# Optimization experiments

Measured on AMD Instinct MI355X. Metric: run time of the kernel, lower is better.

The kernel has to match this reference:

```python
import jax, jax.numpy as jnp
import numpy as np

EPS = 1e-8
LAMBDA_SOFTMAX = 9.0   # opt.lambda_softmax (SCAN t2i default)
ITERATION_STEP = 2     # opt.iteration_step
LEAKY_SLOPE = 0.1      # clipped_l2norm leaky relu slope


def l2norm(x, axis):
    norm = jnp.sqrt(jnp.sum(x * x, axis=axis, keepdims=True)) + EPS
    return x / norm


def cosine_sim(a, b, axis):
    w12 = jnp.sum(a * b, axis=axis)
    w1 = jnp.linalg.norm(a, axis=axis)
    w2 = jnp.linalg.norm(b, axis=axis)
    return w12 / jnp.clip(w1 * w2, EPS)


def func_attention_t2i(query, context):
    """query: [C, I, T, D] caption words per (caption, image) pair;
    context: [I, R, D] image regions. Returns weightedContext [C, I, T, D]."""
    # attn = bmm(context, query^T) -> [C, I, R, T]
    attn = jnp.einsum('ird,citd->cirt', context, query)
    # raw_feature_norm == 'clipped_l2norm': LeakyReLU(0.1) then l2norm over queryL
    attn = jax.nn.leaky_relu(attn, LEAKY_SLOPE)
    attn = l2norm(attn, axis=-1)
    # transpose -> [C, I, T, R]; temperature softmax over sourceL (regions)
    attn = jnp.swapaxes(attn, -1, -2)
    attn = jax.nn.softmax(attn * LAMBDA_SOFTMAX, axis=-1)
    # weightedContext = bmm(context^T, attn^T)^T -> [C, I, T, D]
    return jnp.einsum('citr,ird->citd', attn, context)


def setup_inputs() -> dict:
    key = jax.random.key(0)
    ks = jax.random.split(key, 4)
    B, R, T, D = 32, 36, 40, 1024
    # encoder outputs are l2-normalized along the feature dim
    img_emb = l2norm(jax.random.normal(ks[0], (B, R, D), jnp.float32), axis=-1)
    cap_emb = l2norm(jax.random.normal(ks[1], (B, T, D), jnp.float32), axis=-1)
    W_lin = jax.random.normal(ks[2], (2 * D, D), jnp.float32) * 0.02
    b_lin = jnp.zeros((D,), jnp.float32)
    W_gate = jax.random.normal(ks[3], (2 * D, D), jnp.float32) * 0.02
    b_gate = jnp.zeros((D,), jnp.float32)
    return dict(img_emb=img_emb, cap_emb=cap_emb,
                W_lin=W_lin, b_lin=b_lin, W_gate=W_gate, b_gate=b_gate)


def reference(img_emb, cap_emb, W_lin, b_lin, W_gate, b_gate):
    """xattn_score_Text_IMRAM (t2i) with gated memory, summed over iterations.
    Returns similarity score matrix [n_image, n_caption]."""
    C, T, D = cap_emb.shape
    I = img_emb.shape[0]
    # cap_i_expand: each caption repeated across all images
    cap_exp = jnp.broadcast_to(cap_emb[:, None], (C, I, T, D))
    query = cap_exp
    score = jnp.zeros((I, C), cap_emb.dtype)
    for _ in range(ITERATION_STEP):
        wc = func_attention_t2i(query, img_emb)            # [C, I, T, D]
        # cosine similarity per word vs original caption words, mean over words
        row_sim = cosine_sim(cap_exp, wc, axis=-1).mean(-1)  # [C, I]
        score = score + row_sim.T                           # [I, C]
        # gated_memory_t2i
        cat = jnp.concatenate([query, wc], axis=-1)         # [C, I, T, 2D]
        upd = jnp.tanh(cat @ W_lin + b_lin)
        gate = jax.nn.sigmoid(cat @ W_gate + b_gate)
        query = query * gate + upd * (1.0 - gate)
    return score
```

## Files before the change

kernel.cpp:

```cpp
#include <hip/hip_runtime.h>
#include <stdint.h>


typedef unsigned short u16;
typedef __attribute__((ext_vector_type(8))) short bf16x8;
typedef __attribute__((ext_vector_type(4))) float f32x4;

#define MFMA_BF16(a, b, c) __builtin_amdgcn_mfma_f32_16x16x32_bf16((a), (b), (c), 0, 0, 0)

__device__ __forceinline__ float bf2f(u16 u) {
  union { unsigned v; float f; } x; x.v = ((unsigned)u) << 16; return x.f;
}
__device__ __forceinline__ u16 f2bf(float f) {
  union { float f; unsigned v; } x; x.f = f;
  return (u16)((x.v + 0x7fffu + ((x.v >> 16) & 1u)) >> 16);
}
__device__ __forceinline__ float frcp(float x) { return __builtin_amdgcn_rcpf(x); }
__device__ __forceinline__ void gl2lds16(const u16* g, u16* l) {
  __builtin_amdgcn_global_load_lds((const __attribute__((address_space(1))) void*)g,
                                   (__attribute__((address_space(3))) void*)l, 16, 0, 0);
}

__global__ void prep_k(const float* __restrict__ img, const float* __restrict__ cap,
                       const float* __restrict__ Wl, const float* __restrict__ Wg,
                       u16* __restrict__ imgb, u16* __restrict__ capb,
                       u16* __restrict__ WTl, u16* __restrict__ WTg,
                       float* __restrict__ cnorm, u16* __restrict__ cwT0) {
  __shared__ u16 tile[32][33];
  const int b = blockIdx.x, tid = threadIdx.x;
  if (b < 2432) {
    const float* src; u16* dst; int idx;
    if (b < 1152) { src = img; dst = imgb; idx = (b * 256 + tid) * 4; }
    else { src = cap; dst = capb; idx = ((b - 1152) * 256 + tid) * 4; }
    const float4 v = *(const float4*)(src + idx);
    u16 o[4] = {f2bf(v.x), f2bf(v.y), f2bf(v.z), f2bf(v.w)};
    *(uint2*)(dst + idx) = *(const uint2*)o;
  } else if (b < 6528) {
    const int b2 = b - 2432;
    const int bx = b2 & 63, by = (b2 >> 6) & 31, bz = b2 >> 11;
    const float* src = bz ? Wg : Wl;
    u16* dst = bz ? WTg : WTl;
    const int k0 = bx * 32, n0 = by * 32;
    const int tx = tid & 31, ty = tid >> 5;
#pragma unroll
    for (int j = 0; j < 4; ++j)
      tile[ty + 8 * j][tx] = f2bf(src[(size_t)(k0 + ty + 8 * j) * 1024 + n0 + tx]);
    __syncthreads();
#pragma unroll
    for (int j = 0; j < 4; ++j)
      dst[(size_t)(n0 + ty + 8 * j) * 2048 + k0 + tx] = tile[tx][ty + 8 * j];
  } else if (b < 6848) {
    const int wv = tid >> 6, lane = tid & 63;
    const int row = (b - 6528) * 4 + wv;
    const float* p = cap + ((size_t)row << 10) + lane * 16;
    float s = 0.f;
#pragma unroll
    for (int e = 0; e < 16; ++e) { float v = p[e]; s += v * v; }
#pragma unroll
    for (int off = 32; off > 0; off >>= 1) s += __shfl_down(s, off, 64);
    if (lane == 0) cnorm[row] = sqrtf(s);
  } else {
    const int idx = ((b - 6848) * 256 + tid) * 8;
    uint4 z; z.x = z.y = z.z = z.w = 0u;
    *(uint4*)(cwT0 + idx) = z;
  }
}

__global__ __launch_bounds__(256, 2) void gemms_k(
    const u16* __restrict__ capb, const u16* __restrict__ imgb,
    const u16* __restrict__ WTl, const u16* __restrict__ WTg,
    u16* __restrict__ preL, u16* __restrict__ preG,
    u16* __restrict__ cwTL, u16* __restrict__ cwTG,
    const float* __restrict__ bL, const float* __restrict__ bG,
    float* __restrict__ S1, u16* __restrict__ Ghi, u16* __restrict__ Glo) {
  __shared__ __align__(16) char lsU[20480];
  const int bid = blockIdx.x;
  const int tid = threadIdx.x;
  const int wv = tid >> 6, lane = tid & 63;
  const int quad = lane >> 4, l15 = lane & 15;
  const bf16x8 zero8 = {0, 0, 0, 0, 0, 0, 0, 0};

  if (bid < 640) {
    u16* lsA = (u16*)lsU;
    u16* lsB = (u16*)(lsU + 4096);
    const int i = bid & 31, m0 = (bid >> 5) * 64;
    const u16* B = imgb + (size_t)i * 36 * 1024;
    f32x4 acc[3];
#pragma unroll
    for (int b = 0; b < 3; ++b) acc[b] = (f32x4){0.f, 0.f, 0.f, 0.f};
    for (int kt = 0; kt < 32; ++kt) {
      if (kt) __syncthreads();
      const int rr = tid >> 2, j = tid & 3;
      const int js = j ^ ((rr >> 2) & 3);
      gl2lds16(capb + (size_t)(m0 + rr) * 1024 + kt * 32 + js * 8,
               lsA + (size_t)(wv * 64) * 8);
      const int rc = rr < 36 ? rr : 35;
      gl2lds16(B + (size_t)rc * 1024 + kt * 32 + js * 8,
               lsB + (size_t)(wv * 64) * 8);
      __syncthreads();
      const int ra = wv * 16 + l15;
      const bf16x8 a2 = *(const bf16x8*)(lsA + ra * 32 + (quad ^ ((ra >> 2) & 3)) * 8);
      bf16x8 b3[3];
#pragma unroll
      for (int nf = 0; nf < 3; ++nf) {
        const int rb = nf * 16 + l15;
        const bf16x8 bv = *(const bf16x8*)(lsB + rb * 32 + (quad ^ ((rb >> 2) & 3)) * 8);
        b3[nf] = (rb < 36) ? bv : zero8;
      }
#pragma unroll
      for (int nf = 0; nf < 3; ++nf) acc[nf] = MFMA_BF16(a2, b3[nf], acc[nf]);
    }
#pragma unroll
    for (int nf = 0; nf < 3; ++nf)
#pragma unroll
      for (int rg = 0; rg < 4; ++rg) {
        const int m = m0 + wv * 16 + quad * 4 + rg;
        S1[((size_t)i * 1280 + m) * 48 + nf * 16 + l15] = acc[nf][rg];
      }
  } else if (bid < 944) {
    u16* lsA = (u16*)lsU;
    u16* lsBl = (u16*)(lsU + 4096);
    u16* lsBg = (u16*)(lsU + 12288);
    const int b2 = bid - 640;
    const int bm = b2 >> 3, bn = b2 & 7;
    const bool iscap = bm < 20;
    const u16* A = iscap ? capb + (size_t)bm * 64 * 1024
                         : imgb + (size_t)(bm - 20) * 64 * 1024;
    const int kofs = iscap ? 0 : 1024;
    const int wm = (wv & 1) * 32, wn = (wv >> 1) * 64;
    f32x4 accL[2][4], accG[2][4];
#pragma unroll
    for (int a = 0; a < 2; ++a)
#pragma unroll
      for (int b = 0; b < 4; ++b) {
        accL[a][b] = (f32x4){0.f, 0.f, 0.f, 0.f};
        accG[a][b] = (f32x4){0.f, 0.f, 0.f, 0.f};
      }
    for (int kt = 0; kt < 32; ++kt) {
      if (kt) __syncthreads();
      {
        const int row = tid >> 2, c8 = tid & 3;
        const int js = c8 ^ (row & 3);
        gl2lds16(A + (size_t)row * 1024 + kt * 32 + js * 8,
                 lsA + (size_t)(wv * 64) * 8);
      }
#pragma unroll
      for (int s = 0; s < 2; ++s) {
        const int idx = s * 256 + tid;
        const int row = idx >> 2, c8 = idx & 3;
        const int js = c8 ^ (row & 3);
        const size_t bro = (size_t)(bn * 128 + row) * 2048 + kofs + kt * 32 + js * 8;
        gl2lds16(WTl + bro, lsBl + (size_t)(s * 256 + wv * 64) * 8);
        gl2lds16(WTg + bro, lsBg + (size_t)(s * 256 + wv * 64) * 8);
      }
      __syncthreads();
      bf16x8 af[2], bl8[4], bg8[4];
#pragma unroll
      for (int mt = 0; mt < 2; ++mt) {
        const int ra = wm + mt * 16 + l15;
        af[mt] = *(const bf16x8*)(lsA + ra * 32 + (quad ^ (ra & 3)) * 8);
      }
#pragma unroll
      for (int nt = 0; nt < 4; ++nt) {
        const int rb = wn + nt * 16 + l15;
        const int off = rb * 32 + (quad ^ (rb & 3)) * 8;
        bl8[nt] = *(const bf16x8*)(lsBl + off);
        bg8[nt] = *(const bf16x8*)(lsBg + off);
      }
#pragma unroll
      for (int mt = 0; mt < 2; ++mt)
#pragma unroll
        for (int nt = 0; nt < 4; ++nt) {
          accL[mt][nt] = MFMA_BF16(af[mt], bl8[nt], accL[mt][nt]);
          accG[mt][nt] = MFMA_BF16(af[mt], bg8[nt], accG[mt][nt]);
        }
    }
#pragma unroll
    for (int mt = 0; mt < 2; ++mt)
#pragma unroll
      for (int nt = 0; nt < 4; ++nt) {
        const int n = bn * 128 + wn + nt * 16 + l15;
        if (iscap) {
          const float blv = bL[n], bgv = bG[n];
#pragma unroll
          for (int r = 0; r < 4; ++r) {
            const int m = bm * 64 + wm + mt * 16 + quad * 4 + r;
            preL[((size_t)m << 10) + n] = f2bf(accL[mt][nt][r] + blv);
            preG[((size_t)m << 10) + n] = f2bf(accG[mt][nt][r] + bgv);
          }
        } else {
#pragma unroll
          for (int r = 0; r < 4; ++r) {
            const int mi = (bm - 20) * 64 + wm + mt * 16 + quad * 4 + r;
            const int i = (mi * 3641) >> 17;
            const int r36 = mi - i * 36;
            const size_t gb = (((size_t)(i << 10)) + n) * 64 + r36;
            cwTL[gb] = f2bf(accL[mt][nt][r]);
            cwTG[gb] = f2bf(accG[mt][nt][r]);
          }
        }
      }
  } else {
    float* lsS = (float*)lsU;
    const int i = bid - 944;
    for (int k = tid; k < 48 * 52; k += 256) lsS[k] = 0.f;
    const u16* arow[3]; bool avalid[3];
#pragma unroll
    for (int mt = 0; mt < 3; ++mt) {
      const int r = mt * 16 + l15;
      avalid[mt] = r < 36;
      arow[mt] = imgb + ((size_t)(i * 36 + (r < 36 ? r : 35)) << 10);
    }
    f32x4 acc[3][3];
#pragma unroll
    for (int a = 0; a < 3; ++a)
#pragma unroll
      for (int b = 0; b < 3; ++b) acc[a][b] = (f32x4){0.f, 0.f, 0.f, 0.f};
    for (int kk = wv * 8; kk < wv * 8 + 8; ++kk) {
      const int ko = kk * 32 + quad * 8;
      bf16x8 af[3];
#pragma unroll
      for (int mt = 0; mt < 3; ++mt)
        af[mt] = avalid[mt] ? *(const bf16x8*)(arow[mt] + ko) : zero8;
#pragma unroll
      for (int mt = 0; mt < 3; ++mt)
#pragma unroll
        for (int nt = 0; nt < 3; ++nt)
          acc[mt][nt] = MFMA_BF16(af[mt], af[nt], acc[mt][nt]);
    }
    __syncthreads();
#pragma unroll
    for (int mt = 0; mt < 3; ++mt)
#pragma unroll
      for (int nt = 0; nt < 3; ++nt)
#pragma unroll
        for (int rg = 0; rg < 4; ++rg)
          atomicAdd(&lsS[(nt * 16 + l15) * 52 + mt * 16 + quad * 4 + rg],
                    acc[mt][nt][rg]);
    __syncthreads();
    if (wv == 0) {
#pragma unroll
      for (int nt = 0; nt < 3; ++nt) {
        const int rp = nt * 16 + l15;
#pragma unroll
        for (int mt = 0; mt < 3; ++mt) {
          const f32x4 g = *(const f32x4*)&lsS[rp * 52 + mt * 16 + quad * 4];
          u16 hv[4], lv[4];
#pragma unroll
          for (int rg = 0; rg < 4; ++rg) {
            hv[rg] = f2bf(g[rg]);
            lv[rg] = f2bf(g[rg] - bf2f(hv[rg]));
          }
          const size_t gb = ((size_t)i * 48 + rp) * 64 + mt * 16 + quad * 4;
          *(uint2*)(Ghi + gb) = *(const uint2*)hv;
          *(uint2*)(Glo + gb) = *(const uint2*)lv;
        }
      }
    }
    for (int k = tid; k < 48 * 16; k += 256) {
      const size_t gb = ((size_t)i * 48 + (k >> 4)) * 64 + 48 + (k & 15);
      Ghi[gb] = 0; Glo[gb] = 0;
    }
  }
}

__global__ __launch_bounds__(256, 4) void gates2_k(
    const u16* __restrict__ cwTL, const u16* __restrict__ cwTG,
    const u16* __restrict__ P1, const u16* __restrict__ preL,
    const u16* __restrict__ preG, const u16* __restrict__ capb,
    const u16* __restrict__ imgb, float* __restrict__ S2) {
  __shared__ __align__(16) u16 lsPre[3][32 * 128];
  __shared__ __align__(16) float lsS2f[32 * 52];
  const int tid = threadIdx.x;
  const int bid = blockIdx.x;
  const int i = bid & 31, ctt = bid >> 5;
  const int ct0 = ctt * 32;
  const int wv = tid >> 6, lane = tid & 63;
  const int quad = lane >> 4, l15 = lane & 15;

  for (int k = tid; k < 32 * 52; k += 256) lsS2f[k] = 0.f;

  bf16x8 bp[2][2];
#pragma unroll
  for (int nt = 0; nt < 2; ++nt)
#pragma unroll
    for (int ks = 0; ks < 2; ++ks)
      bp[nt][ks] = *(const bf16x8*)(
          P1 + ((size_t)i * 1280 + ct0 + nt * 16 + l15) * 64 + ks * 32 + quad * 8);

  const u16* arow[3]; bool avalid[3];
#pragma unroll
  for (int mt = 0; mt < 3; ++mt) {
    const int r = mt * 16 + l15;
    avalid[mt] = r < 36;
    arow[mt] = imgb + ((size_t)(i * 36 + (r < 36 ? r : 35)) << 10);
  }
  const bf16x8 zero8 = {0, 0, 0, 0, 0, 0, 0, 0};

  f32x4 acc2[3][2];
#pragma unroll
  for (int a = 0; a < 3; ++a)
#pragma unroll
    for (int b = 0; b < 2; ++b) acc2[a][b] = (f32x4){0.f, 0.f, 0.f, 0.f};

#define STAGE(dcx)                                                          \
  {                                                                         \
    _Pragma("unroll")                                                       \
    for (int s = 0; s < 2; ++s) {                                           \
      const int idx = s * 256 + tid;                                        \
      const int rr = idx >> 4, j = idx & 15;                                \
      const int js = j ^ (rr & 7);                                          \
      const size_t src = (size_t)(ct0 + rr) * 1024 + (dcx) * 128 + js * 8;  \
      const size_t dst = (size_t)(s * 256 + wv * 64) * 8;                   \
      gl2lds16(preL + src, lsPre[0] + dst);                                 \
      gl2lds16(preG + src, lsPre[1] + dst);                                 \
      gl2lds16(capb + src, lsPre[2] + dst);                                 \
    }                                                                       \
  }

  STAGE(0);
  for (int dc = 0; dc < 8; ++dc) {
    __syncthreads();
    f32x4 accL[2][2], accG[2][2];
#pragma unroll
    for (int a = 0; a < 2; ++a)
#pragma unroll
      for (int b = 0; b < 2; ++b) {
        accL[a][b] = (f32x4){0.f, 0.f, 0.f, 0.f};
        accG[a][b] = (f32x4){0.f, 0.f, 0.f, 0.f};
      }
#pragma unroll
    for (int mt = 0; mt < 2; ++mt)
#pragma unroll
      for (int ks = 0; ks < 2; ++ks) {
        const int ra = dc * 128 + wv * 32 + mt * 16 + l15;
        const size_t co = ((size_t)(i << 10) + ra) * 64 + ks * 32 + quad * 8;
        const bf16x8 al = *(const bf16x8*)(cwTL + co);
        const bf16x8 ag = *(const bf16x8*)(cwTG + co);
#pragma unroll
        for (int nt = 0; nt < 2; ++nt) {
          accL[mt][nt] = MFMA_BF16(al, bp[nt][ks], accL[mt][nt]);
          accG[mt][nt] = MFMA_BF16(ag, bp[nt][ks], accG[mt][nt]);
        }
      }
    uint2 ovv[2][2];
#pragma unroll
    for (int mt = 0; mt < 2; ++mt) {
      const int drel = wv * 32 + mt * 16 + quad * 4;
      const int j = drel >> 3;
#pragma unroll
      for (int nt = 0; nt < 2; ++nt) {
        const int rr = nt * 16 + l15;
        const int off = rr * 128 + (j ^ (rr & 7)) * 8 + (quad & 1) * 4;
        const uint2 plv = *(const uint2*)(lsPre[0] + off);
        const uint2 pgv = *(const uint2*)(lsPre[1] + off);
        const uint2 cfv = *(const uint2*)(lsPre[2] + off);
        const float pl4[4] = {bf2f((u16)(plv.x & 0xffffu)), bf2f((u16)(plv.x >> 16)),
                              bf2f((u16)(plv.y & 0xffffu)), bf2f((u16)(plv.y >> 16))};
        const float pg4[4] = {bf2f((u16)(pgv.x & 0xffffu)), bf2f((u16)(pgv.x >> 16)),
                              bf2f((u16)(pgv.y & 0xffffu)), bf2f((u16)(pgv.y >> 16))};
        const float cf4[4] = {bf2f((u16)(cfv.x & 0xffffu)), bf2f((u16)(cfv.x >> 16)),
                              bf2f((u16)(cfv.y & 0xffffu)), bf2f((u16)(cfv.y >> 16))};
        u16 ov[4];
#pragma unroll
        for (int rg = 0; rg < 4; ++rg) {
          const float aL = accL[mt][nt][rg] + pl4[rg];
          const float aG = accG[mt][nt][rg] + pg4[rg];
          const float g = frcp(1.f + __expf(-aG));
          const float u = 2.f * frcp(1.f + __expf(-2.f * aL)) - 1.f;
          ov[rg] = f2bf(cf4[rg] * g + u * (1.f - g));
        }
        ovv[mt][nt] = *(const uint2*)ov;
      }
    }
    __syncthreads();
    if (dc < 7) STAGE(dc + 1);

#pragma unroll
    for (int nt = 0; nt < 2; ++nt) {
      unsigned w[4];
#pragma unroll
      for (int j2 = 0; j2 < 4; ++j2) {
        const int srcl = ((quad & 1) * 2 + (j2 >> 1)) * 16 + l15;
        const unsigned a0 =
            __shfl((j2 & 1) ? ovv[0][nt].y : ovv[0][nt].x, srcl, 64);
        const unsigned a1 =
            __shfl((j2 & 1) ? ovv[1][nt].y : ovv[1][nt].x, srcl, 64);
        w[j2] = (quad >= 2) ? a1 : a0;
      }
      union { unsigned u[4]; bf16x8 v; } bq;
      bq.u[0] = w[0]; bq.u[1] = w[1]; bq.u[2] = w[2]; bq.u[3] = w[3];
      const int dg = dc * 128 + wv * 32 + quad * 8;
#pragma unroll
      for (int mt = 0; mt < 3; ++mt) {
        const bf16x8 af = avalid[mt] ? *(const bf16x8*)(arow[mt] + dg) : zero8;
        acc2[mt][nt] = MFMA_BF16(af, bq.v, acc2[mt][nt]);
      }
    }
  }
#undef STAGE
#pragma unroll
  for (int mt = 0; mt < 3; ++mt)
#pragma unroll
    for (int nt = 0; nt < 2; ++nt)
#pragma unroll
      for (int rg = 0; rg < 4; ++rg)
        atomicAdd(&lsS2f[(nt * 16 + l15) * 52 + mt * 16 + quad * 4 + rg],
                  acc2[mt][nt][rg]);
  __syncthreads();
  for (int idx = tid; idx < 384; idx += 256) {
    const int ct = idx / 12, rq = idx % 12;
    *(f32x4*)(S2 + ((size_t)i * 1280 + ct0 + ct) * 48 + rq * 4) =
        *(const f32x4*)&lsS2f[ct * 52 + rq * 4];
  }
}

template <int PASS2>
__global__ __launch_bounds__(256, 2) void score_k(
    const float* __restrict__ Ssm, const float* __restrict__ S1,
    const u16* __restrict__ Ghi, const u16* __restrict__ Glo,
    const float* __restrict__ cnorm, u16* __restrict__ P1,
    float* __restrict__ sim1, float* __restrict__ score) {
  __shared__ __align__(16) u16 lsP[4][48 * 72];
  const int tid = threadIdx.x;
  const int wv = tid >> 6, lane = tid & 63;
  const int quad = lane >> 4, l15 = lane & 15;
  const int pair = blockIdx.x * 4 + wv;
  const int c = pair >> 5, i = pair & 31;
  u16* lsPw = lsP[wv];
  for (int k = lane; k < 1728; k += 64) ((unsigned*)lsPw)[k] = 0u;

  float sS[3][3][4], s1f[3][3][4];
  const float* Sb = Ssm + ((size_t)i * 1280 + c * 40) * 48;
  const float* S1b = S1 + ((size_t)i * 1280 + c * 40) * 48;
#pragma unroll
  for (int nt = 0; nt < 3; ++nt) {
    const int t = nt * 16 + l15;
    const int tr = t < 40 ? t : 39;
#pragma unroll
    for (int mt = 0; mt < 3; ++mt) {
      f32x4 v = *(const f32x4*)(Sb + (size_t)tr * 48 + mt * 16 + quad * 4);
      if (t >= 40) v = (f32x4){0.f, 0.f, 0.f, 0.f};
#pragma unroll
      for (int rg = 0; rg < 4; ++rg) sS[mt][nt][rg] = v[rg];
      if (PASS2) {
        const f32x4 w = *(const f32x4*)(S1b + (size_t)tr * 48 + mt * 16 + quad * 4);
#pragma unroll
        for (int rg = 0; rg < 4; ++rg) s1f[mt][nt][rg] = w[rg];
      } else {
#pragma unroll
        for (int rg = 0; rg < 4; ++rg) s1f[mt][nt][rg] = v[rg];
      }
    }
  }

  float rn[3][4];
#pragma unroll
  for (int mt = 0; mt < 3; ++mt)
#pragma unroll
    for (int rg = 0; rg < 4; ++rg) {
      float s2 = 0.f;
#pragma unroll
      for (int nt = 0; nt < 3; ++nt) {
        float v = sS[mt][nt][rg]; v = v > 0.f ? v : 0.1f * v; s2 += v * v;
      }
      s2 += __shfl_xor(s2, 1, 64); s2 += __shfl_xor(s2, 2, 64);
      s2 += __shfl_xor(s2, 4, 64); s2 += __shfl_xor(s2, 8, 64);
      rn[mt][rg] = sqrtf(s2) + 1e-8f;
    }
  float mx[3] = {-3.0e38f, -3.0e38f, -3.0e38f};
#pragma unroll
  for (int mt = 0; mt < 3; ++mt)
#pragma unroll
    for (int nt = 0; nt < 3; ++nt)
#pragma unroll
      for (int rg = 0; rg < 4; ++rg) {
        const int r = mt * 16 + quad * 4 + rg;
        float v = sS[mt][nt][rg]; v = v > 0.f ? v : 0.1f * v;
        float zz = 9.f * v / rn[mt][rg];
        zz = (r < 36) ? zz : -3.0e38f;
        sS[mt][nt][rg] = zz;
        mx[nt] = fmaxf(mx[nt], zz);
      }
#pragma unroll
  for (int nt = 0; nt < 3; ++nt) {
    mx[nt] = fmaxf(mx[nt], __shfl_xor(mx[nt], 16, 64));
    mx[nt] = fmaxf(mx[nt], __shfl_xor(mx[nt], 32, 64));
  }
  float ss[3] = {0.f, 0.f, 0.f};
#pragma unroll
  for (int mt = 0; mt < 3; ++mt)
#pragma unroll
    for (int nt = 0; nt < 3; ++nt)
#pragma unroll
      for (int rg = 0; rg < 4; ++rg) {
        const float e = __expf(sS[mt][nt][rg] - mx[nt]);
        sS[mt][nt][rg] = e; ss[nt] += e;
      }
#pragma unroll
  for (int nt = 0; nt < 3; ++nt) {
    ss[nt] += __shfl_xor(ss[nt], 16, 64);
    ss[nt] += __shfl_xor(ss[nt], 32, 64);
    ss[nt] = 1.f / ss[nt];
  }
#pragma unroll
  for (int nt = 0; nt < 3; ++nt) {
    const int t = nt * 16 + l15;
#pragma unroll
    for (int mt = 0; mt < 3; ++mt) {
#pragma unroll
      for (int rg = 0; rg < 4; ++rg) sS[mt][nt][rg] *= ss[nt];
      if (t < 40) {
        u16 pv[4];
#pragma unroll
        for (int rg = 0; rg < 4; ++rg) pv[rg] = f2bf(sS[mt][nt][rg]);
        *(uint2*)(lsPw + t * 72 + mt * 16 + quad * 4) = *(const uint2*)pv;
      }
    }
  }

  float pnv[3] = {0.f, 0.f, 0.f};
#pragma unroll
  for (int nt = 0; nt < 3; ++nt)
#pragma unroll
    for (int mt = 0; mt < 3; ++mt)
#pragma unroll
      for (int rg = 0; rg < 4; ++rg) pnv[nt] += sS[mt][nt][rg] * s1f[mt][nt][rg];

  if (!PASS2) {
    for (int idx = lane; idx < 320; idx += 64) {
      const int t = idx >> 3, j = idx & 7;
      *(uint4*)(P1 + ((size_t)i * 1280 + c * 40 + t) * 64 + j * 8) =
          *(const uint4*)(lsPw + t * 72 + j * 8);
    }
  }

  bf16x8 afA[3][2];
#pragma unroll
  for (int mtT = 0; mtT < 3; ++mtT)
#pragma unroll
    for (int ks = 0; ks < 2; ++ks)
      afA[mtT][ks] =
          *(const bf16x8*)(lsPw + (mtT * 16 + l15) * 72 + ks * 32 + quad * 8);
  f32x4 gp[3][3];
#pragma unroll
  for (int a = 0; a < 3; ++a)
#pragma unroll
    for (int b = 0; b < 3; ++b) gp[a][b] = (f32x4){0.f, 0.f, 0.f, 0.f};
#pragma unroll
  for (int ks = 0; ks < 2; ++ks)
#pragma unroll
    for (int mtG = 0; mtG < 3; ++mtG) {
      const size_t gb = ((size_t)i * 48 + mtG * 16 + l15) * 64 + ks * 32 + quad * 8;
      const bf16x8 gh = *(const bf16x8*)(Ghi + gb);
      const bf16x8 gl = *(const bf16x8*)(Glo + gb);
#pragma unroll
      for (int mtT = 0; mtT < 3; ++mtT) {
        gp[mtG][mtT] = MFMA_BF16(gh, afA[mtT][ks], gp[mtG][mtT]);
        gp[mtG][mtT] = MFMA_BF16(gl, afA[mtT][ks], gp[mtG][mtT]);
      }
    }
  float pwv[3] = {0.f, 0.f, 0.f};
#pragma unroll
  for (int nt = 0; nt < 3; ++nt)
#pragma unroll
    for (int mt = 0; mt < 3; ++mt)
#pragma unroll
      for (int rg = 0; rg < 4; ++rg)
        pwv[nt] += sS[mt][nt][rg] * gp[mt][nt][rg];
#pragma unroll
  for (int nt = 0; nt < 3; ++nt) {
    pnv[nt] += __shfl_xor(pnv[nt], 16, 64); pnv[nt] += __shfl_xor(pnv[nt], 32, 64);
    pwv[nt] += __shfl_xor(pwv[nt], 16, 64); pwv[nt] += __shfl_xor(pwv[nt], 32, 64);
  }
  float tot = 0.f;
#pragma unroll
  for (int nt = 0; nt < 3; ++nt) {
    const int t = nt * 16 + l15;
    if (t < 40) {
      const float w2 = sqrtf(fmaxf(pwv[nt], 0.f));
      tot += pnv[nt] / fmaxf(cnorm[c * 40 + t] * w2, 1e-8f);
    }
  }
  tot += __shfl_xor(tot, 1, 64); tot += __shfl_xor(tot, 2, 64);
  tot += __shfl_xor(tot, 4, 64); tot += __shfl_xor(tot, 8, 64);
  if (lane == 0) {
    const float s = tot * (1.f / 40.f);
    if (PASS2) score[i * 32 + c] = sim1[pair] + s;
    else sim1[pair] = s;
  }
}

extern "C" void kernel_launch(void* const* d_in, const int* in_sizes, int n_in,
                              void* d_out, int out_size, void* d_ws, size_t ws_size,
                              hipStream_t stream) {
  const float* img = (const float*)d_in[0];
  const float* cap = (const float*)d_in[1];
  const float* Wl  = (const float*)d_in[2];
  const float* bl  = (const float*)d_in[3];
  const float* Wg  = (const float*)d_in[4];
  const float* bg  = (const float*)d_in[5];
  float* out = (float*)d_out;

  char* ws = (char*)d_ws;
  float* cnrm = (float*)ws;               ws += 5120;
  float* sim1 = (float*)ws;               ws += 4096;
  u16*   WTl  = (u16*)ws;                 ws += (size_t)1024 * 2048 * 2;
  u16*   WTg  = (u16*)ws;                 ws += (size_t)1024 * 2048 * 2;
  u16*   preL = (u16*)ws;                 ws += (size_t)1280 * 1024 * 2;
  u16*   preG = (u16*)ws;                 ws += (size_t)1280 * 1024 * 2;
  u16*   capb = (u16*)ws;                 ws += (size_t)1280 * 1024 * 2;
  u16*   imgb = (u16*)ws;                 ws += (size_t)1152 * 1024 * 2;
  u16*   Ghi  = (u16*)ws;                 ws += (size_t)32 * 48 * 64 * 2;
  u16*   Glo  = (u16*)ws;                 ws += (size_t)32 * 48 * 64 * 2;
  u16*   cwTL = (u16*)ws;                 ws += (size_t)32 * 1024 * 64 * 2;
  u16*   cwTG = (u16*)ws;                 ws += (size_t)32 * 1024 * 64 * 2;
  float* S1   = (float*)ws;               ws += (size_t)32 * 1280 * 48 * 4;
  float* S2   = (float*)ws;               ws += (size_t)32 * 1280 * 48 * 4;
  u16*   P1   = (u16*)ws;                 ws += (size_t)32 * 1280 * 64 * 2;

  prep_k<<<8896, 256, 0, stream>>>(img, cap, Wl, Wg, imgb, capb, WTl, WTg,
                                   cnrm, cwTL);
  gemms_k<<<976, 256, 0, stream>>>(capb, imgb, WTl, WTg, preL, preG,
                                   cwTL, cwTG, bl, bg, S1, Ghi, Glo);
  score_k<0><<<256, 256, 0, stream>>>(S1, S1, Ghi, Glo, cnrm, P1, sim1, out);
  gates2_k<<<1280, 256, 0, stream>>>(cwTL, cwTG, P1, preL, preG, capb, imgb, S2);
  score_k<1><<<256, 256, 0, stream>>>(S2, S1, Ghi, Glo, cnrm, P1, sim1, out);
}
```

Measured before the change: 247.4 us.

## Halve gates2 caption tile, double-buffer LDS staging and prefetch cw operands

The gates2 kernel now handles 16 caption tokens per block instead of 32, doubling the grid to 2560 blocks. The staged preL/preG/cap tiles are double-buffered, so the next chunk's global-to-LDS load is issued right after the barrier and one of the two barriers per iteration goes away. The cwTL/cwTG operands for the next chunk are loaded into registers a step ahead, and the image fragments are loaded before the gating math. The aim is more parallelism and better overlap of memory latency, at the cost of re-reading the cw and img operands in twice as many blocks.

```diff
diff --git a/kernel.cpp b/kernel.cpp
--- a/kernel.cpp
+++ b/kernel.cpp
@@ -269,24 +269,22 @@
     const u16* __restrict__ P1, const u16* __restrict__ preL,
     const u16* __restrict__ preG, const u16* __restrict__ capb,
     const u16* __restrict__ imgb, float* __restrict__ S2) {
-  __shared__ __align__(16) u16 lsPre[3][32 * 128];
-  __shared__ __align__(16) float lsS2f[32 * 52];
+  __shared__ __align__(16) u16 lsPre[2][3][16 * 128];
+  __shared__ __align__(16) float lsS2f[16 * 52];
   const int tid = threadIdx.x;
   const int bid = blockIdx.x;
   const int i = bid & 31, ctt = bid >> 5;
-  const int ct0 = ctt * 32;
+  const int ct0 = ctt * 16;
   const int wv = tid >> 6, lane = tid & 63;
   const int quad = lane >> 4, l15 = lane & 15;
 
-  for (int k = tid; k < 32 * 52; k += 256) lsS2f[k] = 0.f;
-
-  bf16x8 bp[2][2];
-#pragma unroll
-  for (int nt = 0; nt < 2; ++nt)
-#pragma unroll
-    for (int ks = 0; ks < 2; ++ks)
-      bp[nt][ks] = *(const bf16x8*)(
-          P1 + ((size_t)i * 1280 + ct0 + nt * 16 + l15) * 64 + ks * 32 + quad * 8);
+  for (int k = tid; k < 16 * 52; k += 256) lsS2f[k] = 0.f;
+
+  bf16x8 bp[2];
+#pragma unroll
+  for (int ks = 0; ks < 2; ++ks)
+    bp[ks] = *(const bf16x8*)(
+        P1 + ((size_t)i * 1280 + ct0 + l15) * 64 + ks * 32 + quad * 8);
 
   const u16* arow[3]; bool avalid[3];
 #pragma unroll
@@ -297,118 +295,120 @@
   }
   const bf16x8 zero8 = {0, 0, 0, 0, 0, 0, 0, 0};
 
-  f32x4 acc2[3][2];
-#pragma unroll
-  for (int a = 0; a < 3; ++a)
-#pragma unroll
-    for (int b = 0; b < 2; ++b) acc2[a][b] = (f32x4){0.f, 0.f, 0.f, 0.f};
-
-#define STAGE(dcx)                                                          \
+  f32x4 acc2[3];
+  acc2[0] = acc2[1] = acc2[2] = (f32x4){0.f, 0.f, 0.f, 0.f};
+
+#define STAGE(dcx, bsel)                                                    \
+  {                                                                         \
+    const int rr = tid >> 4, j = tid & 15;                                  \
+    const int js = j ^ (rr & 7);                                            \
+    const size_t src = (size_t)(ct0 + rr) * 1024 + (dcx) * 128 + js * 8;    \
+    const size_t dst = (size_t)(wv * 64) * 8;                               \
+    gl2lds16(preL + src, lsPre[bsel][0] + dst);                             \
+    gl2lds16(preG + src, lsPre[bsel][1] + dst);                             \
+    gl2lds16(capb + src, lsPre[bsel][2] + dst);                             \
+  }
+
+  bf16x8 cwl[2][2], cwg[2][2];
+#define LOADCW(dcx)                                                         \
   {                                                                         \
     _Pragma("unroll")                                                       \
-    for (int s = 0; s < 2; ++s) {                                           \
-      const int idx = s * 256 + tid;                                        \
-      const int rr = idx >> 4, j = idx & 15;                                \
-      const int js = j ^ (rr & 7);                                          \
-      const size_t src = (size_t)(ct0 + rr) * 1024 + (dcx) * 128 + js * 8;  \
-      const size_t dst = (size_t)(s * 256 + wv * 64) * 8;                   \
-      gl2lds16(preL + src, lsPre[0] + dst);                                 \
-      gl2lds16(preG + src, lsPre[1] + dst);                                 \
-      gl2lds16(capb + src, lsPre[2] + dst);                                 \
-    }                                                                       \
-  }
-
-  STAGE(0);
+    for (int mt = 0; mt < 2; ++mt)                                          \
+      _Pragma("unroll")                                                     \
+      for (int ks = 0; ks < 2; ++ks) {                                      \
+        const int ra = (dcx) * 128 + wv * 32 + mt * 16 + l15;               \
+        const size_t co = ((size_t)(i << 10) + ra) * 64 + ks * 32 + quad * 8; \
+        cwl[mt][ks] = *(const bf16x8*)(cwTL + co);                          \
+        cwg[mt][ks] = *(const bf16x8*)(cwTG + co);                          \
+      }                                                                     \
+  }
+
+  STAGE(0, 0);
+  LOADCW(0);
+
   for (int dc = 0; dc < 8; ++dc) {
     __syncthreads();
-    f32x4 accL[2][2], accG[2][2];
-#pragma unroll
-    for (int a = 0; a < 2; ++a)
-#pragma unroll
-      for (int b = 0; b < 2; ++b) {
-        accL[a][b] = (f32x4){0.f, 0.f, 0.f, 0.f};
-        accG[a][b] = (f32x4){0.f, 0.f, 0.f, 0.f};
-      }
+    if (dc < 7) STAGE(dc + 1, (dc + 1) & 1);
+
+    f32x4 accL[2], accG[2];
+#pragma unroll
+    for (int a = 0; a < 2; ++a) {
+      accL[a] = (f32x4){0.f, 0.f, 0.f, 0.f};
+      accG[a] = (f32x4){0.f, 0.f, 0.f, 0.f};
+    }
 #pragma unroll
     for (int mt = 0; mt < 2; ++mt)
 #pragma unroll
       for (int ks = 0; ks < 2; ++ks) {
-        const int ra = dc * 128 + wv * 32 + mt * 16 + l15;
-        const size_t co = ((size_t)(i << 10) + ra) * 64 + ks * 32 + quad * 8;
-        const bf16x8 al = *(const bf16x8*)(cwTL + co);
-        const bf16x8 ag = *(const bf16x8*)(cwTG + co);
-#pragma unroll
-        for (int nt = 0; nt < 2; ++nt) {
-          accL[mt][nt] = MFMA_BF16(al, bp[nt][ks], accL[mt][nt]);
-          accG[mt][nt] = MFMA_BF16(ag, bp[nt][ks], accG[mt][nt]);
-        }
-      }
-    uint2 ovv[2][2];
+        accL[mt] = MFMA_BF16(cwl[mt][ks], bp[ks], accL[mt]);
+        accG[mt] = MFMA_BF16(cwg[mt][ks], bp[ks], accG[mt]);
+      }
+    if (dc < 7) LOADCW(dc + 1);
+
+    bf16x8 af3[3];
+    {
+      const int dg = dc * 128 + wv * 32 + quad * 8;
+#pragma unroll
+      for (int mt = 0; mt < 3; ++mt)
+        af3[mt] = avalid[mt] ? *(const bf16x8*)(arow[mt] + dg) : zero8;
+    }
+
+    const u16* lsP0 = lsPre[dc & 1][0];
+    const u16* lsP1 = lsPre[dc & 1][1];
+    const u16* lsP2 = lsPre[dc & 1][2];
+    uint2 ovv[2];
 #pragma unroll
     for (int mt = 0; mt < 2; ++mt) {
       const int drel = wv * 32 + mt * 16 + quad * 4;
       const int j = drel >> 3;
-#pragma unroll
-      for (int nt = 0; nt < 2; ++nt) {
-        const int rr = nt * 16 + l15;
-        const int off = rr * 128 + (j ^ (rr & 7)) * 8 + (quad & 1) * 4;
-        const uint2 plv = *(const uint2*)(lsPre[0] + off);
-        const uint2 pgv = *(const uint2*)(lsPre[1] + off);
-        const uint2 cfv = *(const uint2*)(lsPre[2] + off);
-        const float pl4[4] = {bf2f((u16)(plv.x & 0xffffu)), bf2f((u16)(plv.x >> 16)),
-                              bf2f((u16)(plv.y & 0xffffu)), bf2f((u16)(plv.y >> 16))};
-        const float pg4[4] = {bf2f((u16)(pgv.x & 0xffffu)), bf2f((u16)(pgv.x >> 16)),
-                              bf2f((u16)(pgv.y & 0xffffu)), bf2f((u16)(pgv.y >> 16))};
-        const float cf4[4] = {bf2f((u16)(cfv.x & 0xffffu)), bf2f((u16)(cfv.x >> 16)),
-                              bf2f((u16)(cfv.y & 0xffffu)), bf2f((u16)(cfv.y >> 16))};
-        u16 ov[4];
-#pragma unroll
-        for (int rg = 0; rg < 4; ++rg) {
-          const float aL = accL[mt][nt][rg] + pl4[rg];
-          const float aG = accG[mt][nt][rg] + pg4[rg];
-          const float g = frcp(1.f + __expf(-aG));
-          const float u = 2.f * frcp(1.f + __expf(-2.f * aL)) - 1.f;
-          ov[rg] = f2bf(cf4[rg] * g + u * (1.f - g));
-        }
-        ovv[mt][nt] = *(const uint2*)ov;
-      }
-    }
-    __syncthreads();
-    if (dc < 7) STAGE(dc + 1);
-
-#pragma unroll
-    for (int nt = 0; nt < 2; ++nt) {
+      const int rr = l15;
+      const int off = rr * 128 + (j ^ (rr & 7)) * 8 + (quad & 1) * 4;
+      const uint2 plv = *(const uint2*)(lsP0 + off);
+      const uint2 pgv = *(const uint2*)(lsP1 + off);
+      const uint2 cfv = *(const uint2*)(lsP2 + off);
+      const float pl4[4] = {bf2f((u16)(plv.x & 0xffffu)), bf2f((u16)(plv.x >> 16)),
+                            bf2f((u16)(plv.y & 0xffffu)), bf2f((u16)(plv.y >> 16))};
+      const float pg4[4] = {bf2f((u16)(pgv.x & 0xffffu)), bf2f((u16)(pgv.x >> 16)),
+                            bf2f((u16)(pgv.y & 0xffffu)), bf2f((u16)(pgv.y >> 16))};
+      const float cf4[4] = {bf2f((u16)(cfv.x & 0xffffu)), bf2f((u16)(cfv.x >> 16)),
+                            bf2f((u16)(cfv.y & 0xffffu)), bf2f((u16)(cfv.y >> 16))};
+      u16 ov[4];
+#pragma unroll
+      for (int rg = 0; rg < 4; ++rg) {
+        const float aL = accL[mt][rg] + pl4[rg];
+        const float aG = accG[mt][rg] + pg4[rg];
+        const float g = frcp(1.f + __expf(-aG));
+        const float u = 2.f * frcp(1.f + __expf(-2.f * aL)) - 1.f;
+        ov[rg] = f2bf(cf4[rg] * g + u * (1.f - g));
+      }
+      ovv[mt] = *(const uint2*)ov;
+    }
+
+    {
       unsigned w[4];
 #pragma unroll
       for (int j2 = 0; j2 < 4; ++j2) {
         const int srcl = ((quad & 1) * 2 + (j2 >> 1)) * 16 + l15;
-        const unsigned a0 =
-            __shfl((j2 & 1) ? ovv[0][nt].y : ovv[0][nt].x, srcl, 64);
-        const unsigned a1 =
-            __shfl((j2 & 1) ? ovv[1][nt].y : ovv[1][nt].x, srcl, 64);
+        const unsigned a0 = __shfl((j2 & 1) ? ovv[0].y : ovv[0].x, srcl, 64);
+        const unsigned a1 = __shfl((j2 & 1) ? ovv[1].y : ovv[1].x, srcl, 64);
         w[j2] = (quad >= 2) ? a1 : a0;
       }
       union { unsigned u[4]; bf16x8 v; } bq;
       bq.u[0] = w[0]; bq.u[1] = w[1]; bq.u[2] = w[2]; bq.u[3] = w[3];
-      const int dg = dc * 128 + wv * 32 + quad * 8;
-#pragma unroll
-      for (int mt = 0; mt < 3; ++mt) {
-        const bf16x8 af = avalid[mt] ? *(const bf16x8*)(arow[mt] + dg) : zero8;
-        acc2[mt][nt] = MFMA_BF16(af, bq.v, acc2[mt][nt]);
-      }
+#pragma unroll
+      for (int mt = 0; mt < 3; ++mt)
+        acc2[mt] = MFMA_BF16(af3[mt], bq.v, acc2[mt]);
     }
   }
 #undef STAGE
+#undef LOADCW
 #pragma unroll
   for (int mt = 0; mt < 3; ++mt)
 #pragma unroll
-    for (int nt = 0; nt < 2; ++nt)
-#pragma unroll
-      for (int rg = 0; rg < 4; ++rg)
-        atomicAdd(&lsS2f[(nt * 16 + l15) * 52 + mt * 16 + quad * 4 + rg],
-                  acc2[mt][nt][rg]);
+    for (int rg = 0; rg < 4; ++rg)
+      atomicAdd(&lsS2f[l15 * 52 + mt * 16 + quad * 4 + rg], acc2[mt][rg]);
   __syncthreads();
-  for (int idx = tid; idx < 384; idx += 256) {
+  for (int idx = tid; idx < 192; idx += 256) {
     const int ct = idx / 12, rq = idx % 12;
     *(f32x4*)(S2 + ((size_t)i * 1280 + ct0 + ct) * 48 + rq * 4) =
         *(const f32x4*)&lsS2f[ct * 52 + rq * 4];
@@ -624,6 +624,6 @@
   gemms_k<<<976, 256, 0, stream>>>(capb, imgb, WTl, WTg, preL, preG,
                                    cwTL, cwTG, bl, bg, S1, Ghi, Glo);
   score_k<0><<<256, 256, 0, stream>>>(S1, S1, Ghi, Glo, cnrm, P1, sim1, out);
-  gates2_k<<<1280, 256, 0, stream>>>(cwTL, cwTG, P1, preL, preG, capb, imgb, S2);
+  gates2_k<<<2560, 256, 0, stream>>>(cwTL, cwTG, P1, preL, preG, capb, imgb, S2);
   score_k<1><<<256, 256, 0, stream>>>(S2, S1, Ghi, Glo, cnrm, P1, sim1, out);
 }
```

Measured after the change: 271.2 us. +9.6%, slower.
